# Kernel tuning notes

Measured on AMD Instinct MI355X. Metric: run time of the kernel, lower is better.

The kernel has to match this reference:

```python
import jax, jax.numpy as jnp
import numpy as np


def setup_inputs() -> dict:
    key = jax.random.key(0)
    k1, k2, k3, k4 = jax.random.split(key, 4)
    B, T, F_in, F_out, N, E, K = 16, 64, 64, 64, 128, 2, 4
    x = jax.random.normal(k1, (B, T, F_in, N), dtype=jnp.float32)
    # graph shift operator per (batch, time, edge-feature); scaled to keep powers bounded
    S = jax.random.normal(k2, (B, T, E, N, N), dtype=jnp.float32) / np.sqrt(N)
    H = jax.random.normal(k3, (F_out, E, K, F_in), dtype=jnp.float32) * 0.02
    bias = jax.random.normal(k4, (F_out, 1), dtype=jnp.float32) * 0.02
    return {"x": x, "S": S, "H": H, "bias": bias}


def reference(x, S, H, bias):
    # x: [B,T,F_in,N], S: [B,T,E,N,N], H: [F_out,E,K,F_in], bias: [F_out,1]
    B, T, F_in, N = x.shape
    E = S.shape[2]
    F_out, _, K, _ = H.shape
    # replicate features across edge-feature dim: [B,T,E,F_in,N]
    cur = jnp.broadcast_to(x[:, :, None], (B, T, E, F_in, N))
    taps = [cur]
    zero_row = jnp.zeros((B, 1, E, F_in, N), dtype=x.dtype)
    for _ in range(1, K):
        # time-shift: tap k at time t depends on tap k-1 at time t-1
        cur = jnp.concatenate([zero_row, cur[:, :-1]], axis=1)
        # diffuse over graph: [..,F_in,N] @ [..,N,N]
        cur = jnp.matmul(cur, S)
        taps.append(cur)
    z = jnp.stack(taps, axis=2)  # [B,T,K,E,F_in,N]
    # [B,T,N, E*K*F_in], matching permute(0,1,5,3,2,4) in the source
    z = z.transpose(0, 1, 5, 3, 2, 4).reshape(B, T, N, E * K * F_in)
    Hm = H.reshape(F_out, E * K * F_in)
    y = jnp.einsum('btnf,of->bton', z, Hm)  # [B,T,F_out,N]
    return y + bias  # bias [F_out,1] broadcasts over N
```

## Files before the change

kernel.cpp:

```cpp
#include <hip/hip_runtime.h>


namespace {
constexpr int B = 16, T = 64, F = 64, N = 128, E = 2, K = 4;
constexpr int SSW = 136;
constexpr int SZW = 136;
}

typedef short v8s __attribute__((ext_vector_type(8)));
typedef float v4f __attribute__((ext_vector_type(4)));

__device__ inline ushort f2bf(float f) {
  union { float f; uint u; } v; v.f = f;
  uint u = v.u;
  return (ushort)((u + 0x7fffu + ((u >> 16) & 1u)) >> 16);
}

__device__ inline uint pk2(float a, float b) {
  return (uint)f2bf(a) | ((uint)f2bf(b) << 16);
}

__global__ __launch_bounds__(256) void gf_prep(
    const float* __restrict__ x, const float* __restrict__ H,
    ushort* __restrict__ xT, ushort* __restrict__ Hb) {
  __shared__ ushort tile[64 * 128];
  const int bid = blockIdx.x;
  const int tid = threadIdx.x;
  if (bid < B * T) {
    const float* xg = x + (size_t)bid * F * N;
    ushort* Og = xT + (size_t)bid * N * F;
    #pragma unroll
    for (int it = 0; it < 4; ++it) {
      const int idx = tid + it * 256;
      const int f = idx >> 4, g = idx & 15;
      const float4 v0 = *(const float4*)(xg + f * N + g * 8);
      const float4 v1 = *(const float4*)(xg + f * N + g * 8 + 4);
      uint4 w;
      w.x = pk2(v0.x, v0.y); w.y = pk2(v0.z, v0.w);
      w.z = pk2(v1.x, v1.y); w.w = pk2(v1.z, v1.w);
      const int gp = g ^ (f >> 3);
      *(uint4*)&tile[f * 128 + gp * 8] = w;
    }
    __syncthreads();
    if (tid < 128) {
      const int a = tid & 7, b = tid >> 3;
      v8s rows[8];
      #pragma unroll
      for (int j = 0; j < 8; ++j)
        rows[j] = *(const v8s*)&tile[(8 * a + j) * 128 + ((b ^ a) * 8)];
      #pragma unroll
      for (int i = 0; i < 8; ++i) {
        uint4 w;
        w.x = (uint)(ushort)rows[0][i] | ((uint)(ushort)rows[1][i] << 16);
        w.y = (uint)(ushort)rows[2][i] | ((uint)(ushort)rows[3][i] << 16);
        w.z = (uint)(ushort)rows[4][i] | ((uint)(ushort)rows[5][i] << 16);
        w.w = (uint)(ushort)rows[6][i] | ((uint)(ushort)rows[7][i] << 16);
        *(uint4*)(Og + (8 * b + i) * F + 8 * a) = w;
      }
    }
  } else {
    const int hb = bid - B * T;
    const int d = (hb * 256 + tid) * 4;
    const int f = d & 63, o = (d >> 6) & 63, k = (d >> 12) & 3, e = (d >> 14) & 1;
    const float4 v = *(const float4*)(H + (((size_t)o * E + e) * K + k) * F + f);
    uint2 w;
    w.x = pk2(v.x, v.y);
    w.y = pk2(v.z, v.w);
    *(uint2*)(Hb + d) = w;
  }
}

__global__ __launch_bounds__(256, 3) void gf_chain(
    const float* __restrict__ S, const ushort* __restrict__ xT,
    const ushort* __restrict__ Hb, const float* __restrict__ bias,
    float* __restrict__ y) {
  __shared__ ushort sS[128 * SSW];
  __shared__ ushort sZ[64 * SZW];
  const int bid = blockIdx.x;
  const int t = bid & (T - 1);
  const int tid = threadIdx.x, w = tid >> 6, lane = tid & 63;
  const int l15 = lane & 15, q = lane >> 4;

  v4f yacc[2][4];
  #pragma unroll
  for (int mt = 0; mt < 2; ++mt)
    #pragma unroll
    for (int ot = 0; ot < 4; ++ot) {
      yacc[mt][ot][0] = 0.f; yacc[mt][ot][1] = 0.f;
      yacc[mt][ot][2] = 0.f; yacc[mt][ot][3] = 0.f;
    }

  for (int e = 0; e < E; ++e) {
    v4f acc[2][4];
    bool have = false;
    #pragma unroll
    for (int tap = 3; tap >= 0; --tap) {
      const int s = t - tap;
      if (s < 0) continue;
      const bool doMM = have;
      const float* Sg = S + (size_t)((bid - tap) * E + e) * (N * N);

      if (doMM) {
        __syncthreads();
        #pragma unroll
        for (int mt = 0; mt < 2; ++mt)
          #pragma unroll
          for (int ot = 0; ot < 4; ++ot) {
            uint2 wv;
            wv.x = pk2(acc[mt][ot][0], acc[mt][ot][1]);
            wv.y = pk2(acc[mt][ot][2], acc[mt][ot][3]);
            *(uint2*)&sZ[(ot * 16 + l15) * SZW + (2 * w + mt) * 16 + q * 4] = wv;
          }
        #pragma unroll
        for (int half = 0; half < 2; ++half) {
          float4 r0[4], r1[4];
          #pragma unroll
          for (int it = 0; it < 4; ++it) {
            const int idx = tid + (half * 4 + it) * 256;
            const int m = idx >> 4, g = idx & 15;
            r0[it] = *(const float4*)(Sg + m * N + g * 8);
            r1[it] = *(const float4*)(Sg + m * N + g * 8 + 4);
          }
          #pragma unroll
          for (int it = 0; it < 4; ++it) {
            const int idx = tid + (half * 4 + it) * 256;
            const int m = idx >> 4, g = idx & 15;
            uint4 wv;
            wv.x = pk2(r0[it].x, r0[it].y); wv.y = pk2(r0[it].z, r0[it].w);
            wv.z = pk2(r1[it].x, r1[it].y); wv.w = pk2(r1[it].z, r1[it].w);
            *(uint4*)&sS[m * SSW + ((g ^ (m >> 3)) * 8)] = wv;
          }
        }
      }

      v4f (*tgt)[4] = (tap == 0) ? yacc : acc;
      if (tap != 0) {
        #pragma unroll
        for (int mt = 0; mt < 2; ++mt)
          #pragma unroll
          for (int ot = 0; ot < 4; ++ot) {
            acc[mt][ot][0] = 0.f; acc[mt][ot][1] = 0.f;
            acc[mt][ot][2] = 0.f; acc[mt][ot][3] = 0.f;
          }
      }
      {
        const ushort* xrow = xT + (size_t)(bid - tap) * (N * F);
        const ushort* hbase = Hb + (size_t)((e * K + tap) * 64) * 64;
        v8s xf[2][2], hf[4][2];
        #pragma unroll
        for (int mt = 0; mt < 2; ++mt) {
          const ushort* xr = xrow + ((2 * w + mt) * 16 + l15) * F;
          xf[mt][0] = *(const v8s*)(xr + q * 8);
          xf[mt][1] = *(const v8s*)(xr + 32 + q * 8);
        }
        #pragma unroll
        for (int ot = 0; ot < 4; ++ot) {
          const ushort* hr = hbase + (ot * 16 + l15) * 64;
          hf[ot][0] = *(const v8s*)(hr + q * 8);
          hf[ot][1] = *(const v8s*)(hr + 32 + q * 8);
        }
        #pragma unroll
        for (int fk = 0; fk < 2; ++fk)
          #pragma unroll
          for (int mt = 0; mt < 2; ++mt)
            #pragma unroll
            for (int ot = 0; ot < 4; ++ot)
              tgt[mt][ot] = __builtin_amdgcn_mfma_f32_16x16x32_bf16(
                  xf[mt][fk], hf[ot][fk], tgt[mt][ot], 0, 0, 0);
      }

      if (doMM) {
        __syncthreads();
        const int a = tid & 15, bg = tid >> 4;
        v8s rows[8];
        #pragma unroll
        for (int j = 0; j < 8; ++j)
          rows[j] = *(const v8s*)&sS[(8 * a + j) * SSW + ((bg ^ a) * 8)];
        __syncthreads();
        #pragma unroll
        for (int i = 0; i < 8; ++i) {
          uint4 wv;
          wv.x = (uint)(ushort)rows[0][i] | ((uint)(ushort)rows[1][i] << 16);
          wv.y = (uint)(ushort)rows[2][i] | ((uint)(ushort)rows[3][i] << 16);
          wv.z = (uint)(ushort)rows[4][i] | ((uint)(ushort)rows[5][i] << 16);
          wv.w = (uint)(ushort)rows[6][i] | ((uint)(ushort)rows[7][i] << 16);
          *(uint4*)&sS[(8 * bg + i) * SSW + ((a ^ bg) * 8)] = wv;
        }
        __syncthreads();
        #pragma unroll
        for (int c = 0; c < 4; ++c) {
          v8s bz[4];
          #pragma unroll
          for (int ot = 0; ot < 4; ++ot)
            bz[ot] = *(const v8s*)&sZ[(ot * 16 + l15) * SZW + c * 32 + q * 8];
          #pragma unroll
          for (int mt = 0; mt < 2; ++mt) {
            const int n = (2 * w + mt) * 16 + l15;
            const v8s af = *(const v8s*)&sS[n * SSW + ((((c << 2) | q) ^ (n >> 3)) * 8)];
            #pragma unroll
            for (int ot = 0; ot < 4; ++ot)
              tgt[mt][ot] = __builtin_amdgcn_mfma_f32_16x16x32_bf16(
                  af, bz[ot], tgt[mt][ot], 0, 0, 0);
          }
        }
      }
      have = true;
    }
  }

  float* yg = y + (size_t)bid * (F * N);
  #pragma unroll
  for (int ot = 0; ot < 4; ++ot) {
    const int o = ot * 16 + l15;
    const float bv = bias[o];
    #pragma unroll
    for (int mt = 0; mt < 2; ++mt) {
      float4 v;
      v.x = yacc[mt][ot][0] + bv; v.y = yacc[mt][ot][1] + bv;
      v.z = yacc[mt][ot][2] + bv; v.w = yacc[mt][ot][3] + bv;
      *(float4*)(yg + o * N + (2 * w + mt) * 16 + q * 4) = v;
    }
  }
}

extern "C" void kernel_launch(void* const* d_in, const int* in_sizes, int n_in,
                              void* d_out, int out_size, void* d_ws, size_t ws_size,
                              hipStream_t stream) {
  const float* x    = (const float*)d_in[0];
  const float* S    = (const float*)d_in[1];
  const float* H    = (const float*)d_in[2];
  const float* bias = (const float*)d_in[3];
  float* y = (float*)d_out;

  const size_t XTn = (size_t)B * T * N * F;
  ushort* xT = (ushort*)d_ws;
  ushort* Hb = xT + XTn;

  gf_prep <<<B * T + 32, 256, 0, stream>>>(x, H, xT, Hb);
  gf_chain<<<B * T,      256, 0, stream>>>(S, xT, Hb, bias, y);
}
```

Before: 302.4 us.

## Precompute transposed bf16 S once in prep kernel, drop in-chain transpose

Moves the fp32-to-bf16 conversion and transpose of every S matrix into the prep kernel, which writes a transposed bf16 copy to workspace. The chain kernel then loads MFMA A-fragments for S straight from global memory instead of re-converting and transposing each S up to three times per block through shared memory. The change also double-buffers the sZ staging buffer to remove a barrier, raises the occupancy target to 4 blocks per CU, and swizzles the block index so blocks that share time neighbours run together. The cost is an extra global write and read of bf16 S, plus more global-latency-bound fragment loads inside the chain loop.

Result: slower. 309.5 us (+2.3%).

```diff
diff --git a/kernel.cpp b/kernel.cpp
--- a/kernel.cpp
+++ b/kernel.cpp
@@ -21,9 +21,10 @@
 }
 
 __global__ __launch_bounds__(256) void gf_prep(
-    const float* __restrict__ x, const float* __restrict__ H,
-    ushort* __restrict__ xT, ushort* __restrict__ Hb) {
-  __shared__ ushort tile[64 * 128];
+    const float* __restrict__ x, const float* __restrict__ S,
+    const float* __restrict__ H, ushort* __restrict__ xT,
+    ushort* __restrict__ Hb, ushort* __restrict__ ST) {
+  __shared__ ushort sh[128 * SSW];
   const int bid = blockIdx.x;
   const int tid = threadIdx.x;
   if (bid < B * T) {
@@ -35,11 +36,11 @@
       const int f = idx >> 4, g = idx & 15;
       const float4 v0 = *(const float4*)(xg + f * N + g * 8);
       const float4 v1 = *(const float4*)(xg + f * N + g * 8 + 4);
-      uint4 w;
-      w.x = pk2(v0.x, v0.y); w.y = pk2(v0.z, v0.w);
-      w.z = pk2(v1.x, v1.y); w.w = pk2(v1.z, v1.w);
+      uint4 wv;
+      wv.x = pk2(v0.x, v0.y); wv.y = pk2(v0.z, v0.w);
+      wv.z = pk2(v1.x, v1.y); wv.w = pk2(v1.z, v1.w);
       const int gp = g ^ (f >> 3);
-      *(uint4*)&tile[f * 128 + gp * 8] = w;
+      *(uint4*)&sh[f * 128 + gp * 8] = wv;
     }
     __syncthreads();
     if (tid < 128) {
@@ -47,36 +48,75 @@
       v8s rows[8];
       #pragma unroll
       for (int j = 0; j < 8; ++j)
-        rows[j] = *(const v8s*)&tile[(8 * a + j) * 128 + ((b ^ a) * 8)];
+        rows[j] = *(const v8s*)&sh[(8 * a + j) * 128 + ((b ^ a) * 8)];
       #pragma unroll
       for (int i = 0; i < 8; ++i) {
-        uint4 w;
-        w.x = (uint)(ushort)rows[0][i] | ((uint)(ushort)rows[1][i] << 16);
-        w.y = (uint)(ushort)rows[2][i] | ((uint)(ushort)rows[3][i] << 16);
-        w.z = (uint)(ushort)rows[4][i] | ((uint)(ushort)rows[5][i] << 16);
-        w.w = (uint)(ushort)rows[6][i] | ((uint)(ushort)rows[7][i] << 16);
-        *(uint4*)(Og + (8 * b + i) * F + 8 * a) = w;
-      }
-    }
-  } else {
+        uint4 wv;
+        wv.x = (uint)(ushort)rows[0][i] | ((uint)(ushort)rows[1][i] << 16);
+        wv.y = (uint)(ushort)rows[2][i] | ((uint)(ushort)rows[3][i] << 16);
+        wv.z = (uint)(ushort)rows[4][i] | ((uint)(ushort)rows[5][i] << 16);
+        wv.w = (uint)(ushort)rows[6][i] | ((uint)(ushort)rows[7][i] << 16);
+        *(uint4*)(Og + (8 * b + i) * F + 8 * a) = wv;
+      }
+    }
+  } else if (bid < B * T + 32) {
     const int hb = bid - B * T;
     const int d = (hb * 256 + tid) * 4;
     const int f = d & 63, o = (d >> 6) & 63, k = (d >> 12) & 3, e = (d >> 14) & 1;
     const float4 v = *(const float4*)(H + (((size_t)o * E + e) * K + k) * F + f);
-    uint2 w;
-    w.x = pk2(v.x, v.y);
-    w.y = pk2(v.z, v.w);
-    *(uint2*)(Hb + d) = w;
+    uint2 wv;
+    wv.x = pk2(v.x, v.y);
+    wv.y = pk2(v.z, v.w);
+    *(uint2*)(Hb + d) = wv;
+  } else {
+    const int sid = bid - (B * T + 32);
+    const float* Sg = S + (size_t)sid * (N * N);
+    ushort* Og = ST + (size_t)sid * (N * N);
+    #pragma unroll
+    for (int half = 0; half < 2; ++half) {
+      float4 r0[4], r1[4];
+      #pragma unroll
+      for (int it = 0; it < 4; ++it) {
+        const int idx = tid + (half * 4 + it) * 256;
+        const int m = idx >> 4, g = idx & 15;
+        r0[it] = *(const float4*)(Sg + m * N + g * 8);
+        r1[it] = *(const float4*)(Sg + m * N + g * 8 + 4);
+      }
+      #pragma unroll
+      for (int it = 0; it < 4; ++it) {
+        const int idx = tid + (half * 4 + it) * 256;
+        const int m = idx >> 4, g = idx & 15;
+        uint4 wv;
+        wv.x = pk2(r0[it].x, r0[it].y); wv.y = pk2(r0[it].z, r0[it].w);
+        wv.z = pk2(r1[it].x, r1[it].y); wv.w = pk2(r1[it].z, r1[it].w);
+        *(uint4*)&sh[m * SSW + ((g ^ (m >> 3)) * 8)] = wv;
+      }
+    }
+    __syncthreads();
+    const int a = tid & 15, bg = tid >> 4;
+    v8s rows[8];
+    #pragma unroll
+    for (int j = 0; j < 8; ++j)
+      rows[j] = *(const v8s*)&sh[(8 * a + j) * SSW + ((bg ^ a) * 8)];
+    #pragma unroll
+    for (int i = 0; i < 8; ++i) {
+      uint4 wv;
+      wv.x = (uint)(ushort)rows[0][i] | ((uint)(ushort)rows[1][i] << 16);
+      wv.y = (uint)(ushort)rows[2][i] | ((uint)(ushort)rows[3][i] << 16);
+      wv.z = (uint)(ushort)rows[4][i] | ((uint)(ushort)rows[5][i] << 16);
+      wv.w = (uint)(ushort)rows[6][i] | ((uint)(ushort)rows[7][i] << 16);
+      *(uint4*)(Og + (8 * bg + i) * N + 8 * a) = wv;
+    }
   }
 }
 
-__global__ __launch_bounds__(256, 3) void gf_chain(
-    const float* __restrict__ S, const ushort* __restrict__ xT,
+__global__ __launch_bounds__(256, 4) void gf_chain(
+    const ushort* __restrict__ ST, const ushort* __restrict__ xT,
     const ushort* __restrict__ Hb, const float* __restrict__ bias,
     float* __restrict__ y) {
-  __shared__ ushort sS[128 * SSW];
-  __shared__ ushort sZ[64 * SZW];
-  const int bid = blockIdx.x;
+  __shared__ ushort sZ[2][64 * SZW];
+  const int bid0 = blockIdx.x;
+  const int bid = ((bid0 & 7) << 7) | (bid0 >> 3);
   const int t = bid & (T - 1);
   const int tid = threadIdx.x, w = tid >> 6, lane = tid & 63;
   const int l15 = lane & 15, q = lane >> 4;
@@ -90,6 +130,7 @@
       yacc[mt][ot][2] = 0.f; yacc[mt][ot][3] = 0.f;
     }
 
+  int pb = 0;
   for (int e = 0; e < E; ++e) {
     v4f acc[2][4];
     bool have = false;
@@ -98,10 +139,8 @@
       const int s = t - tap;
       if (s < 0) continue;
       const bool doMM = have;
-      const float* Sg = S + (size_t)((bid - tap) * E + e) * (N * N);
 
       if (doMM) {
-        __syncthreads();
         #pragma unroll
         for (int mt = 0; mt < 2; ++mt)
           #pragma unroll
@@ -109,28 +148,8 @@
             uint2 wv;
             wv.x = pk2(acc[mt][ot][0], acc[mt][ot][1]);
             wv.y = pk2(acc[mt][ot][2], acc[mt][ot][3]);
-            *(uint2*)&sZ[(ot * 16 + l15) * SZW + (2 * w + mt) * 16 + q * 4] = wv;
+            *(uint2*)&sZ[pb][(ot * 16 + l15) * SZW + (2 * w + mt) * 16 + q * 4] = wv;
           }
-        #pragma unroll
-        for (int half = 0; half < 2; ++half) {
-          float4 r0[4], r1[4];
-          #pragma unroll
-          for (int it = 0; it < 4; ++it) {
-            const int idx = tid + (half * 4 + it) * 256;
-            const int m = idx >> 4, g = idx & 15;
-            r0[it] = *(const float4*)(Sg + m * N + g * 8);
-            r1[it] = *(const float4*)(Sg + m * N + g * 8 + 4);
-          }
-          #pragma unroll
-          for (int it = 0; it < 4; ++it) {
-            const int idx = tid + (half * 4 + it) * 256;
-            const int m = idx >> 4, g = idx & 15;
-            uint4 wv;
-            wv.x = pk2(r0[it].x, r0[it].y); wv.y = pk2(r0[it].z, r0[it].w);
-            wv.z = pk2(r1[it].x, r1[it].y); wv.w = pk2(r1[it].z, r1[it].w);
-            *(uint4*)&sS[m * SSW + ((g ^ (m >> 3)) * 8)] = wv;
-          }
-        }
       }
 
       v4f (*tgt)[4] = (tap == 0) ? yacc : acc;
@@ -146,63 +165,50 @@
       {
         const ushort* xrow = xT + (size_t)(bid - tap) * (N * F);
         const ushort* hbase = Hb + (size_t)((e * K + tap) * 64) * 64;
-        v8s xf[2][2], hf[4][2];
-        #pragma unroll
-        for (int mt = 0; mt < 2; ++mt) {
-          const ushort* xr = xrow + ((2 * w + mt) * 16 + l15) * F;
-          xf[mt][0] = *(const v8s*)(xr + q * 8);
-          xf[mt][1] = *(const v8s*)(xr + 32 + q * 8);
-        }
-        #pragma unroll
-        for (int ot = 0; ot < 4; ++ot) {
-          const ushort* hr = hbase + (ot * 16 + l15) * 64;
-          hf[ot][0] = *(const v8s*)(hr + q * 8);
-          hf[ot][1] = *(const v8s*)(hr + 32 + q * 8);
-        }
-        #pragma unroll
-        for (int fk = 0; fk < 2; ++fk)
+        #pragma unroll
+        for (int fk = 0; fk < 2; ++fk) {
+          v8s xfk[2], hfk[4];
+          #pragma unroll
+          for (int mt = 0; mt < 2; ++mt)
+            xfk[mt] = *(const v8s*)(xrow + ((2 * w + mt) * 16 + l15) * F + fk * 32 + q * 8);
+          #pragma unroll
+          for (int ot = 0; ot < 4; ++ot)
+            hfk[ot] = *(const v8s*)(hbase + (ot * 16 + l15) * 64 + fk * 32 + q * 8);
           #pragma unroll
           for (int mt = 0; mt < 2; ++mt)
             #pragma unroll
             for (int ot = 0; ot < 4; ++ot)
               tgt[mt][ot] = __builtin_amdgcn_mfma_f32_16x16x32_bf16(
-                  xf[mt][fk], hf[ot][fk], tgt[mt][ot], 0, 0, 0);
+                  xfk[mt], hfk[ot], tgt[mt][ot], 0, 0, 0);
+        }
       }
 
       if (doMM) {
+        const ushort* STg = ST + (size_t)((bid - tap) * E + e) * (N * N);
+        const ushort* sr0 = STg + ((2 * w) * 16 + l15) * N + q * 8;
+        const ushort* sr1 = STg + ((2 * w + 1) * 16 + l15) * N + q * 8;
+        v8s af[2][2];
+        af[0][0] = *(const v8s*)sr0;
+        af[0][1] = *(const v8s*)sr1;
         __syncthreads();
-        const int a = tid & 15, bg = tid >> 4;
-        v8s rows[8];
-        #pragma unroll
-        for (int j = 0; j < 8; ++j)
-          rows[j] = *(const v8s*)&sS[(8 * a + j) * SSW + ((bg ^ a) * 8)];
-        __syncthreads();
-        #pragma unroll
-        for (int i = 0; i < 8; ++i) {
-          uint4 wv;
-          wv.x = (uint)(ushort)rows[0][i] | ((uint)(ushort)rows[1][i] << 16);
-          wv.y = (uint)(ushort)rows[2][i] | ((uint)(ushort)rows[3][i] << 16);
-          wv.z = (uint)(ushort)rows[4][i] | ((uint)(ushort)rows[5][i] << 16);
-          wv.w = (uint)(ushort)rows[6][i] | ((uint)(ushort)rows[7][i] << 16);
-          *(uint4*)&sS[(8 * bg + i) * SSW + ((a ^ bg) * 8)] = wv;
-        }
-        __syncthreads();
         #pragma unroll
         for (int c = 0; c < 4; ++c) {
+          if (c < 3) {
+            af[(c + 1) & 1][0] = *(const v8s*)(sr0 + (c + 1) * 32);
+            af[(c + 1) & 1][1] = *(const v8s*)(sr1 + (c + 1) * 32);
+          }
           v8s bz[4];
           #pragma unroll
           for (int ot = 0; ot < 4; ++ot)
-            bz[ot] = *(const v8s*)&sZ[(ot * 16 + l15) * SZW + c * 32 + q * 8];
-          #pragma unroll
-          for (int mt = 0; mt < 2; ++mt) {
-            const int n = (2 * w + mt) * 16 + l15;
-            const v8s af = *(const v8s*)&sS[n * SSW + ((((c << 2) | q) ^ (n >> 3)) * 8)];
+            bz[ot] = *(const v8s*)&sZ[pb][(ot * 16 + l15) * SZW + c * 32 + q * 8];
+          #pragma unroll
+          for (int mt = 0; mt < 2; ++mt)
             #pragma unroll
             for (int ot = 0; ot < 4; ++ot)
               tgt[mt][ot] = __builtin_amdgcn_mfma_f32_16x16x32_bf16(
-                  af, bz[ot], tgt[mt][ot], 0, 0, 0);
-          }
+                  af[c & 1][mt], bz[ot], tgt[mt][ot], 0, 0, 0);
         }
+        pb ^= 1;
       }
       have = true;
     }
@@ -233,9 +239,11 @@
   float* y = (float*)d_out;
 
   const size_t XTn = (size_t)B * T * N * F;
+  const size_t HBn = (size_t)E * K * F * F;
   ushort* xT = (ushort*)d_ws;
   ushort* Hb = xT + XTn;
-
-  gf_prep <<<B * T + 32, 256, 0, stream>>>(x, H, xT, Hb);
-  gf_chain<<<B * T,      256, 0, stream>>>(S, xT, Hb, bias, y);
-}
+  ushort* ST = Hb + HBn;
+
+  gf_prep <<<B * T + 32 + B * T * E, 256, 0, stream>>>(x, S, H, xT, Hb, ST);
+  gf_chain<<<B * T,                  256, 0, stream>>>(ST, xT, Hb, bias, y);
+}
```

## Fuse prep into a time-chunked recurrent kernel carrying diffusion state across steps

Applied to the files above, without the earlier changes.

Replaces the prep and per-timestep chain kernels with one fused kernel. Each block handles a batch, an 8-step time chunk and a 16-wide output-feature slice. It applies H before diffusing, Horner-style, and carries the partial states P/Q/U3 in shared memory across timesteps. Each S matrix is loaded once per timestep per block instead of once per tap, and x and H are converted to bf16 inside the kernel. In exchange, the four output slices each reload the same S, a 3-step halo is recomputed per chunk, blocks are mapped to XCDs by hand, and the time loop runs serially inside each block.

New measurement: 335.1 us. 1.11x slower.

```diff
diff --git a/kernel.cpp b/kernel.cpp
--- a/kernel.cpp
+++ b/kernel.cpp
@@ -4,7 +4,9 @@
 namespace {
 constexpr int B = 16, T = 64, F = 64, N = 128, E = 2, K = 4;
 constexpr int SSW = 136;
+constexpr int SXW = 68;
 constexpr int SZW = 136;
+constexpr int TC = 8;
 }
 
 typedef short v8s __attribute__((ext_vector_type(8)));
@@ -20,162 +22,145 @@
   return (uint)f2bf(a) | ((uint)f2bf(b) << 16);
 }
 
-__global__ __launch_bounds__(256) void gf_prep(
-    const float* __restrict__ x, const float* __restrict__ H,
-    ushort* __restrict__ xT, ushort* __restrict__ Hb) {
-  __shared__ ushort tile[64 * 128];
-  const int bid = blockIdx.x;
-  const int tid = threadIdx.x;
-  if (bid < B * T) {
-    const float* xg = x + (size_t)bid * F * N;
-    ushort* Og = xT + (size_t)bid * N * F;
-    #pragma unroll
-    for (int it = 0; it < 4; ++it) {
-      const int idx = tid + it * 256;
-      const int f = idx >> 4, g = idx & 15;
-      const float4 v0 = *(const float4*)(xg + f * N + g * 8);
-      const float4 v1 = *(const float4*)(xg + f * N + g * 8 + 4);
-      uint4 w;
-      w.x = pk2(v0.x, v0.y); w.y = pk2(v0.z, v0.w);
-      w.z = pk2(v1.x, v1.y); w.w = pk2(v1.z, v1.w);
-      const int gp = g ^ (f >> 3);
-      *(uint4*)&tile[f * 128 + gp * 8] = w;
-    }
-    __syncthreads();
-    if (tid < 128) {
-      const int a = tid & 7, b = tid >> 3;
-      v8s rows[8];
-      #pragma unroll
-      for (int j = 0; j < 8; ++j)
-        rows[j] = *(const v8s*)&tile[(8 * a + j) * 128 + ((b ^ a) * 8)];
-      #pragma unroll
-      for (int i = 0; i < 8; ++i) {
-        uint4 w;
-        w.x = (uint)(ushort)rows[0][i] | ((uint)(ushort)rows[1][i] << 16);
-        w.y = (uint)(ushort)rows[2][i] | ((uint)(ushort)rows[3][i] << 16);
-        w.z = (uint)(ushort)rows[4][i] | ((uint)(ushort)rows[5][i] << 16);
-        w.w = (uint)(ushort)rows[6][i] | ((uint)(ushort)rows[7][i] << 16);
-        *(uint4*)(Og + (8 * b + i) * F + 8 * a) = w;
-      }
-    }
-  } else {
-    const int hb = bid - B * T;
-    const int d = (hb * 256 + tid) * 4;
-    const int f = d & 63, o = (d >> 6) & 63, k = (d >> 12) & 3, e = (d >> 14) & 1;
-    const float4 v = *(const float4*)(H + (((size_t)o * E + e) * K + k) * F + f);
-    uint2 w;
-    w.x = pk2(v.x, v.y);
-    w.y = pk2(v.z, v.w);
-    *(uint2*)(Hb + d) = w;
-  }
-}
-
-__global__ __launch_bounds__(256, 3) void gf_chain(
-    const float* __restrict__ S, const ushort* __restrict__ xT,
-    const ushort* __restrict__ Hb, const float* __restrict__ bias,
+__global__ __launch_bounds__(256, 2) void gf_fused(
+    const float* __restrict__ x, const float* __restrict__ S,
+    const float* __restrict__ H, const float* __restrict__ bias,
     float* __restrict__ y) {
   __shared__ ushort sS[128 * SSW];
-  __shared__ ushort sZ[64 * SZW];
-  const int bid = blockIdx.x;
-  const int t = bid & (T - 1);
+  __shared__ ushort sX[128 * SXW];
+  __shared__ ushort sSt[6][16 * SZW];
+  const int g = blockIdx.x;
+  const int xcd = g & 7, loc = g >> 3;
+  const int os = loc & 3, unitL = loc >> 2;
+  const int unit = xcd * 16 + unitL;
+  const int b = unit >> 3, chunk = unit & 7;
+  const int t0 = chunk * TC;
+  const int ob = os * 16;
   const int tid = threadIdx.x, w = tid >> 6, lane = tid & 63;
   const int l15 = lane & 15, q = lane >> 4;
 
-  v4f yacc[2][4];
-  #pragma unroll
-  for (int mt = 0; mt < 2; ++mt)
-    #pragma unroll
-    for (int ot = 0; ot < 4; ++ot) {
-      yacc[mt][ot][0] = 0.f; yacc[mt][ot][1] = 0.f;
-      yacc[mt][ot][2] = 0.f; yacc[mt][ot][3] = 0.f;
+  for (int i = tid; i < 6 * 16 * SZW; i += 256) ((ushort*)sSt)[i] = 0;
+
+  v4f Yac[2];
+  Yac[0][0] = 0.f; Yac[0][1] = 0.f; Yac[0][2] = 0.f; Yac[0][3] = 0.f;
+  Yac[1] = Yac[0];
+
+  const int tstart = (t0 == 0) ? 0 : t0 - 3;
+  for (int t = tstart; t < t0 + TC; ++t) {
+    const bool skipS = (t0 != 0) && (t == t0 - 3);
+    const bool emit = (t >= t0);
+
+    {
+      const float* xg = x + (size_t)(b * T + t) * (F * N);
+      float4 r0[4], r1[4];
+      #pragma unroll
+      for (int it = 0; it < 4; ++it) {
+        const int idx = tid + it * 256;
+        const int m = idx >> 4, g2 = idx & 15;
+        r0[it] = *(const float4*)(xg + m * N + g2 * 8);
+        r1[it] = *(const float4*)(xg + m * N + g2 * 8 + 4);
+      }
+      #pragma unroll
+      for (int it = 0; it < 4; ++it) {
+        const int idx = tid + it * 256;
+        const int m = idx >> 4, g2 = idx & 15;
+        uint4 wv;
+        wv.x = pk2(r0[it].x, r0[it].y); wv.y = pk2(r0[it].z, r0[it].w);
+        wv.z = pk2(r1[it].x, r1[it].y); wv.w = pk2(r1[it].z, r1[it].w);
+        *(uint4*)&sS[m * SSW + ((g2 ^ (m >> 3)) * 8)] = wv;
+      }
+      __syncthreads();
+      const int bb = tid & 7, a2 = (tid >> 3) & 15, hh = tid >> 7;
+      v8s rows[8];
+      #pragma unroll
+      for (int j = 0; j < 8; ++j)
+        rows[j] = *(const v8s*)&sS[(8 * bb + j) * SSW + ((a2 ^ bb) * 8)];
+      #pragma unroll
+      for (int i = 0; i < 4; ++i) {
+        const int e2 = 4 * hh + i;
+        const int n = 8 * a2 + e2;
+        uint4 wv;
+        wv.x = (uint)(ushort)rows[0][e2] | ((uint)(ushort)rows[1][e2] << 16);
+        wv.y = (uint)(ushort)rows[2][e2] | ((uint)(ushort)rows[3][e2] << 16);
+        wv.z = (uint)(ushort)rows[4][e2] | ((uint)(ushort)rows[5][e2] << 16);
+        wv.w = (uint)(ushort)rows[6][e2] | ((uint)(ushort)rows[7][e2] << 16);
+        *(uint4*)&sX[n * SXW + 8 * bb] = wv;
+      }
+      __syncthreads();
     }
 
-  for (int e = 0; e < E; ++e) {
-    v4f acc[2][4];
-    bool have = false;
-    #pragma unroll
-    for (int tap = 3; tap >= 0; --tap) {
-      const int s = t - tap;
-      if (s < 0) continue;
-      const bool doMM = have;
-      const float* Sg = S + (size_t)((bid - tap) * E + e) * (N * N);
-
-      if (doMM) {
-        __syncthreads();
-        #pragma unroll
-        for (int mt = 0; mt < 2; ++mt)
-          #pragma unroll
-          for (int ot = 0; ot < 4; ++ot) {
-            uint2 wv;
-            wv.x = pk2(acc[mt][ot][0], acc[mt][ot][1]);
-            wv.y = pk2(acc[mt][ot][2], acc[mt][ot][3]);
-            *(uint2*)&sZ[(ot * 16 + l15) * SZW + (2 * w + mt) * 16 + q * 4] = wv;
-          }
+    for (int e = 0; e < E; ++e) {
+      if (!skipS) {
+        const float* Sg = S + (size_t)((b * T + t) * E + e) * (N * N);
         #pragma unroll
         for (int half = 0; half < 2; ++half) {
           float4 r0[4], r1[4];
           #pragma unroll
           for (int it = 0; it < 4; ++it) {
             const int idx = tid + (half * 4 + it) * 256;
-            const int m = idx >> 4, g = idx & 15;
-            r0[it] = *(const float4*)(Sg + m * N + g * 8);
-            r1[it] = *(const float4*)(Sg + m * N + g * 8 + 4);
+            const int m = idx >> 4, g2 = idx & 15;
+            r0[it] = *(const float4*)(Sg + m * N + g2 * 8);
+            r1[it] = *(const float4*)(Sg + m * N + g2 * 8 + 4);
           }
           #pragma unroll
           for (int it = 0; it < 4; ++it) {
             const int idx = tid + (half * 4 + it) * 256;
-            const int m = idx >> 4, g = idx & 15;
+            const int m = idx >> 4, g2 = idx & 15;
             uint4 wv;
             wv.x = pk2(r0[it].x, r0[it].y); wv.y = pk2(r0[it].z, r0[it].w);
             wv.z = pk2(r1[it].x, r1[it].y); wv.w = pk2(r1[it].z, r1[it].w);
-            *(uint4*)&sS[m * SSW + ((g ^ (m >> 3)) * 8)] = wv;
-          }
-        }
-      }
-
-      v4f (*tgt)[4] = (tap == 0) ? yacc : acc;
-      if (tap != 0) {
+            *(uint4*)&sS[m * SSW + ((g2 ^ (m >> 3)) * 8)] = wv;
+          }
+        }
+      }
+
+      v4f Pn[2], Qn[2], U3n[2];
+      #pragma unroll
+      for (int mt = 0; mt < 2; ++mt) {
+        Pn[mt][0] = 0.f; Pn[mt][1] = 0.f; Pn[mt][2] = 0.f; Pn[mt][3] = 0.f;
+        Qn[mt] = Pn[mt]; U3n[mt] = Pn[mt];
+      }
+      {
+        const float* hrow = H + ((size_t)(ob + l15) * E + e) * K * F;
+        v8s xf[2][2];
         #pragma unroll
         for (int mt = 0; mt < 2; ++mt)
           #pragma unroll
-          for (int ot = 0; ot < 4; ++ot) {
-            acc[mt][ot][0] = 0.f; acc[mt][ot][1] = 0.f;
-            acc[mt][ot][2] = 0.f; acc[mt][ot][3] = 0.f;
-          }
-      }
-      {
-        const ushort* xrow = xT + (size_t)(bid - tap) * (N * F);
-        const ushort* hbase = Hb + (size_t)((e * K + tap) * 64) * 64;
-        v8s xf[2][2], hf[4][2];
-        #pragma unroll
-        for (int mt = 0; mt < 2; ++mt) {
-          const ushort* xr = xrow + ((2 * w + mt) * 16 + l15) * F;
-          xf[mt][0] = *(const v8s*)(xr + q * 8);
-          xf[mt][1] = *(const v8s*)(xr + 32 + q * 8);
-        }
-        #pragma unroll
-        for (int ot = 0; ot < 4; ++ot) {
-          const ushort* hr = hbase + (ot * 16 + l15) * 64;
-          hf[ot][0] = *(const v8s*)(hr + q * 8);
-          hf[ot][1] = *(const v8s*)(hr + 32 + q * 8);
-        }
-        #pragma unroll
-        for (int fk = 0; fk < 2; ++fk)
-          #pragma unroll
-          for (int mt = 0; mt < 2; ++mt)
+          for (int fk = 0; fk < 2; ++fk)
+            xf[mt][fk] = *(const v8s*)&sX[((2 * w + mt) * 16 + l15) * SXW +
+                                          fk * 32 + q * 8];
+        #pragma unroll
+        for (int k = 0; k < 4; ++k) {
+          if (k == 0 && !emit) continue;
+          v8s hf[2];
+          #pragma unroll
+          for (int fk = 0; fk < 2; ++fk) {
+            const int f0 = fk * 32 + q * 8;
+            const float4 h0 = *(const float4*)(hrow + k * F + f0);
+            const float4 h1 = *(const float4*)(hrow + k * F + f0 + 4);
+            uint4 u;
+            u.x = pk2(h0.x, h0.y); u.y = pk2(h0.z, h0.w);
+            u.z = pk2(h1.x, h1.y); u.w = pk2(h1.z, h1.w);
+            union { uint4 u; v8s s; } cv; cv.u = u;
+            hf[fk] = cv.s;
+          }
+          v4f* tgt = (k == 0) ? Yac : (k == 1 ? Pn : (k == 2 ? Qn : U3n));
+          #pragma unroll
+          for (int fk = 0; fk < 2; ++fk)
             #pragma unroll
-            for (int ot = 0; ot < 4; ++ot)
-              tgt[mt][ot] = __builtin_amdgcn_mfma_f32_16x16x32_bf16(
-                  xf[mt][fk], hf[ot][fk], tgt[mt][ot], 0, 0, 0);
-      }
-
-      if (doMM) {
+            for (int mt = 0; mt < 2; ++mt)
+              tgt[mt] = __builtin_amdgcn_mfma_f32_16x16x32_bf16(
+                  xf[mt][fk], hf[fk], tgt[mt], 0, 0, 0);
+        }
+      }
+
+      if (!skipS) {
         __syncthreads();
-        const int a = tid & 15, bg = tid >> 4;
+        const int a2 = tid & 15, bg = tid >> 4;
         v8s rows[8];
         #pragma unroll
         for (int j = 0; j < 8; ++j)
-          rows[j] = *(const v8s*)&sS[(8 * a + j) * SSW + ((bg ^ a) * 8)];
+          rows[j] = *(const v8s*)&sS[(8 * a2 + j) * SSW + ((bg ^ a2) * 8)];
         __syncthreads();
         #pragma unroll
         for (int i = 0; i < 8; ++i) {
@@ -184,41 +169,60 @@
           wv.y = (uint)(ushort)rows[2][i] | ((uint)(ushort)rows[3][i] << 16);
           wv.z = (uint)(ushort)rows[4][i] | ((uint)(ushort)rows[5][i] << 16);
           wv.w = (uint)(ushort)rows[6][i] | ((uint)(ushort)rows[7][i] << 16);
-          *(uint4*)&sS[(8 * bg + i) * SSW + ((a ^ bg) * 8)] = wv;
+          *(uint4*)&sS[(8 * bg + i) * SSW + ((a2 ^ bg) * 8)] = wv;
         }
         __syncthreads();
         #pragma unroll
         for (int c = 0; c < 4; ++c) {
-          v8s bz[4];
-          #pragma unroll
-          for (int ot = 0; ot < 4; ++ot)
-            bz[ot] = *(const v8s*)&sZ[(ot * 16 + l15) * SZW + c * 32 + q * 8];
+          const int p = ((4 * c + q) + 2 * l15) & 15;
+          const int sbase = l15 * SZW + p * 8;
+          const v8s bzP = *(const v8s*)&sSt[e * 3 + 0][sbase];
+          const v8s bzQ = *(const v8s*)&sSt[e * 3 + 1][sbase];
+          const v8s bzU = *(const v8s*)&sSt[e * 3 + 2][sbase];
           #pragma unroll
           for (int mt = 0; mt < 2; ++mt) {
             const int n = (2 * w + mt) * 16 + l15;
-            const v8s af = *(const v8s*)&sS[n * SSW + ((((c << 2) | q) ^ (n >> 3)) * 8)];
-            #pragma unroll
-            for (int ot = 0; ot < 4; ++ot)
-              tgt[mt][ot] = __builtin_amdgcn_mfma_f32_16x16x32_bf16(
-                  af, bz[ot], tgt[mt][ot], 0, 0, 0);
-          }
-        }
-      }
-      have = true;
-    }
-  }
-
-  float* yg = y + (size_t)bid * (F * N);
-  #pragma unroll
-  for (int ot = 0; ot < 4; ++ot) {
-    const int o = ot * 16 + l15;
-    const float bv = bias[o];
-    #pragma unroll
-    for (int mt = 0; mt < 2; ++mt) {
-      float4 v;
-      v.x = yacc[mt][ot][0] + bv; v.y = yacc[mt][ot][1] + bv;
-      v.z = yacc[mt][ot][2] + bv; v.w = yacc[mt][ot][3] + bv;
-      *(float4*)(yg + o * N + (2 * w + mt) * 16 + q * 4) = v;
+            const v8s af = *(const v8s*)&sS[n * SSW +
+                                            ((((c << 2) | q) ^ (n >> 3)) * 8)];
+            if (emit)
+              Yac[mt] = __builtin_amdgcn_mfma_f32_16x16x32_bf16(
+                  af, bzP, Yac[mt], 0, 0, 0);
+            Pn[mt] = __builtin_amdgcn_mfma_f32_16x16x32_bf16(
+                af, bzQ, Pn[mt], 0, 0, 0);
+            Qn[mt] = __builtin_amdgcn_mfma_f32_16x16x32_bf16(
+                af, bzU, Qn[mt], 0, 0, 0);
+          }
+        }
+      }
+
+      __syncthreads();
+      #pragma unroll
+      for (int mt = 0; mt < 2; ++mt) {
+        const int cc = (2 * w + mt) * 2 + (q >> 1), h = q & 1;
+        const int p = (cc + 2 * l15) & 15;
+        const int base = l15 * SZW + p * 8 + h * 4;
+        uint2 wv;
+        wv.x = pk2(Pn[mt][0], Pn[mt][1]); wv.y = pk2(Pn[mt][2], Pn[mt][3]);
+        *(uint2*)&sSt[e * 3 + 0][base] = wv;
+        wv.x = pk2(Qn[mt][0], Qn[mt][1]); wv.y = pk2(Qn[mt][2], Qn[mt][3]);
+        *(uint2*)&sSt[e * 3 + 1][base] = wv;
+        wv.x = pk2(U3n[mt][0], U3n[mt][1]); wv.y = pk2(U3n[mt][2], U3n[mt][3]);
+        *(uint2*)&sSt[e * 3 + 2][base] = wv;
+      }
+
+      if (e == 1 && emit) {
+        float* yg = y + (size_t)(b * T + t) * (F * N);
+        const float bv = bias[ob + l15];
+        #pragma unroll
+        for (int mt = 0; mt < 2; ++mt) {
+          float4 v;
+          v.x = Yac[mt][0] + bv; v.y = Yac[mt][1] + bv;
+          v.z = Yac[mt][2] + bv; v.w = Yac[mt][3] + bv;
+          *(float4*)(yg + (ob + l15) * N + (2 * w + mt) * 16 + q * 4) = v;
+          Yac[mt][0] = 0.f; Yac[mt][1] = 0.f;
+          Yac[mt][2] = 0.f; Yac[mt][3] = 0.f;
+        }
+      }
     }
   }
 }
@@ -231,11 +235,7 @@
   const float* H    = (const float*)d_in[2];
   const float* bias = (const float*)d_in[3];
   float* y = (float*)d_out;
-
-  const size_t XTn = (size_t)B * T * N * F;
-  ushort* xT = (ushort*)d_ws;
-  ushort* Hb = xT + XTn;
-
-  gf_prep <<<B * T + 32, 256, 0, stream>>>(x, H, xT, Hb);
-  gf_chain<<<B * T,      256, 0, stream>>>(S, xT, Hb, bias, y);
-}
+  (void)d_ws; (void)ws_size;
+
+  gf_fused<<<512, 256, 0, stream>>>(x, S, H, bias, y);
+}
```
